# Kernel optimization log

Hardware: AMD Instinct MI355X
Metric: run time of the kernel (lower is better)

Reference implementation:

```python
import jax, jax.numpy as jnp
import numpy as np


def setup_inputs() -> dict:
    key = jax.random.key(0)
    k1, k2 = jax.random.split(key)
    x = jax.random.normal(k1, (32, 256, 56, 56), dtype=jnp.float32)
    conv_w = jax.random.normal(k2, (1, 2, 7, 7), dtype=jnp.float32) * 0.1
    return {"x": x, "conv_w": conv_w}


def reference(x, conv_w):
    # channel-wise mean and max, keepdim -> [B,1,H,W] each
    avg_out = jnp.mean(x, axis=1, keepdims=True)
    max_out = jnp.max(x, axis=1, keepdims=True)
    y = jnp.concatenate([avg_out, max_out], axis=1)  # [B,2,H,W]
    pad = (conv_w.shape[-1] - 1) // 2
    y = jax.lax.conv_general_dilated(
        y, conv_w,
        window_strides=(1, 1),
        padding=[(pad, pad), (pad, pad)],
        dimension_numbers=("NCHW", "OIHW", "NCHW"),
    )  # [B,1,H,W]
    y = jax.nn.sigmoid(y)
    return x * y
```

## Files before the change

### kernel.cpp

```cpp
#include <hip/hip_runtime.h>
#include <math.h>

#define BN   32
#define CN   256
#define HN   56
#define WN   56
#define HWN  (HN * WN)
#define HW4  (HWN / 4)
#define CHW4 (CN * HW4)
#define CHWN (CN * HWN)
#define NPOS (BN * HWN)
#define NQ   (NPOS / 4)

typedef float f32x4 __attribute__((ext_vector_type(4)));

__global__ __launch_bounds__(512) void sa_reduce_kernel(const f32x4* __restrict__ x4,
                                                        f32x4* __restrict__ avg4,
                                                        f32x4* __restrict__ mx4) {
    __shared__ f32x4 s_sum[16][32];
    __shared__ f32x4 s_max[16][32];

    int t    = threadIdx.x;
    int lane = t & 63;
    int w    = t >> 6;
    int j    = lane & 31;
    int sub  = lane >> 5;

    int q  = blockIdx.x * 32 + j;
    int b  = q / HW4;
    int s4 = q - b * HW4;
    const f32x4* xp = x4 + (size_t)b * CHW4 + (size_t)(w * 32 + sub) * HW4 + s4;

    f32x4 sum = {0.0f, 0.0f, 0.0f, 0.0f};
    f32x4 m   = {-INFINITY, -INFINITY, -INFINITY, -INFINITY};
#pragma unroll
    for (int k = 0; k < 16; ++k) {
        f32x4 v = xp[(size_t)(2 * k) * HW4];
        sum += v;
        m.x = fmaxf(m.x, v.x);
        m.y = fmaxf(m.y, v.y);
        m.z = fmaxf(m.z, v.z);
        m.w = fmaxf(m.w, v.w);
    }
    s_sum[w * 2 + sub][j] = sum;
    s_max[w * 2 + sub][j] = m;
    __syncthreads();

    if (t < 32) {
        f32x4 sa = s_sum[0][t];
        f32x4 ma = s_max[0][t];
#pragma unroll
        for (int p = 1; p < 16; ++p) {
            sa += s_sum[p][t];
            f32x4 mp = s_max[p][t];
            ma.x = fmaxf(ma.x, mp.x);
            ma.y = fmaxf(ma.y, mp.y);
            ma.z = fmaxf(ma.z, mp.z);
            ma.w = fmaxf(ma.w, mp.w);
        }
        int qq = blockIdx.x * 32 + t;
        avg4[qq] = sa * (1.0f / (float)CN);
        mx4[qq]  = ma;
    }
}

__global__ __launch_bounds__(256) void sa_conv_kernel(const float* __restrict__ avg,
                                                      const float* __restrict__ mx,
                                                      const float* __restrict__ cw,
                                                      float* __restrict__ att) {
    int p = blockIdx.x * blockDim.x + threadIdx.x;
    if (p >= NPOS) return;
    int b = p / HWN;
    int s = p - b * HWN;
    int h = s / WN;
    int w = s - h * WN;
    const float* a0 = avg + b * HWN;
    const float* m0 = mx + b * HWN;
    float acc = 0.0f;
#pragma unroll
    for (int kh = 0; kh < 7; ++kh) {
        int hh = h + kh - 3;
        if (hh < 0 || hh >= HN) continue;
#pragma unroll
        for (int kw = 0; kw < 7; ++kw) {
            int ww = w + kw - 3;
            if (ww < 0 || ww >= WN) continue;
            int idx = hh * WN + ww;
            acc = fmaf(cw[kh * 7 + kw],      a0[idx], acc);
            acc = fmaf(cw[49 + kh * 7 + kw], m0[idx], acc);
        }
    }
    att[p] = 1.0f / (1.0f + expf(-acc));
}

__global__ __launch_bounds__(256) void sa_mul_kernel(const f32x4* __restrict__ x4,
                                                     const f32x4* __restrict__ att4,
                                                     f32x4* __restrict__ out4) {
    int b = blockIdx.y;
    int i = blockIdx.x * 256 + threadIdx.x;
    int sq = i % HW4;
    f32x4 a = att4[(size_t)b * HW4 + sq];
    size_t gi = (size_t)b * CHW4 + i;
    f32x4 v = x4[gi];
    v *= a;
    __builtin_nontemporal_store(v, out4 + gi);
}

extern "C" void kernel_launch(void* const* d_in, const int* in_sizes, int n_in,
                              void* d_out, int out_size, void* d_ws, size_t ws_size,
                              hipStream_t stream) {
    const float* x  = (const float*)d_in[0];
    const float* cw = (const float*)d_in[1];
    float* out = (float*)d_out;

    float* avg = (float*)d_ws;
    float* mx  = avg + NPOS;
    float* att = mx + NPOS;

    {
        sa_reduce_kernel<<<NQ / 32, 512, 0, stream>>>(
            (const f32x4*)x, (f32x4*)avg, (f32x4*)mx);
    }
    {
        int blocks = (NPOS + 255) / 256;
        sa_conv_kernel<<<blocks, 256, 0, stream>>>(avg, mx, cw, att);
    }
    {
        dim3 grid(CHW4 / 256, BN);
        sa_mul_kernel<<<grid, 256, 0, stream>>>(
            (const f32x4*)x, (const f32x4*)att, (f32x4*)out);
    }
}
```

Measured before the change: 203.2 us.

## Fuse reduce, conv and multiply into one cooperative persistent kernel

Replaces three kernel launches with a single cooperative kernel of 784 blocks that performs the channel reduction, then a grid sync, the 7x7 conv plus sigmoid, then another grid sync, and finally the scaling multiply. Each block re-reads the same x positions it reduced, so the multiply pass may hit in L2 or the large last-level cache. This removes launch gaps between kernels. In exchange it adds two grid-wide barriers, and it needs all 784 blocks of 256 threads resident at once, which the 4-blocks-per-CU launch bound is meant to allow.

```diff
diff --git a/kernel.cpp b/kernel.cpp
--- a/kernel.cpp
+++ b/kernel.cpp
@@ -1,5 +1,8 @@
 #include <hip/hip_runtime.h>
+#include <hip/hip_cooperative_groups.h>
 #include <math.h>
+
+namespace cg = cooperative_groups;
 
 #define BN   32
 #define CN   256
@@ -11,14 +14,20 @@
 #define CHWN (CN * HWN)
 #define NPOS (BN * HWN)
 #define NQ   (NPOS / 4)
+#define GRID 784
 
 typedef float f32x4 __attribute__((ext_vector_type(4)));
 
-__global__ __launch_bounds__(512) void sa_reduce_kernel(const f32x4* __restrict__ x4,
-                                                        f32x4* __restrict__ avg4,
-                                                        f32x4* __restrict__ mx4) {
-    __shared__ f32x4 s_sum[16][32];
-    __shared__ f32x4 s_max[16][32];
+__global__ __launch_bounds__(256, 4) void sa_fused_kernel(
+    const f32x4* __restrict__ x4,
+    const float* __restrict__ cw,
+    f32x4*       __restrict__ out4,
+    float*       __restrict__ avg,
+    float*       __restrict__ mx,
+    float*       __restrict__ att)
+{
+    __shared__ f32x4 s_sum[8][32];
+    __shared__ f32x4 s_max[8][32];
 
     int t    = threadIdx.x;
     int lane = t & 63;
@@ -29,13 +38,13 @@
     int q  = blockIdx.x * 32 + j;
     int b  = q / HW4;
     int s4 = q - b * HW4;
-    const f32x4* xp = x4 + (size_t)b * CHW4 + (size_t)(w * 32 + sub) * HW4 + s4;
+    size_t xbase = (size_t)b * CHW4 + (size_t)(w * 64 + sub) * HW4 + s4;
 
     f32x4 sum = {0.0f, 0.0f, 0.0f, 0.0f};
     f32x4 m   = {-INFINITY, -INFINITY, -INFINITY, -INFINITY};
-#pragma unroll
-    for (int k = 0; k < 16; ++k) {
-        f32x4 v = xp[(size_t)(2 * k) * HW4];
+#pragma unroll 8
+    for (int k = 0; k < 32; ++k) {
+        f32x4 v = x4[xbase + (size_t)(2 * k) * HW4];
         sum += v;
         m.x = fmaxf(m.x, v.x);
         m.y = fmaxf(m.y, v.y);
@@ -50,7 +59,7 @@
         f32x4 sa = s_sum[0][t];
         f32x4 ma = s_max[0][t];
 #pragma unroll
-        for (int p = 1; p < 16; ++p) {
+        for (int p = 1; p < 8; ++p) {
             sa += s_sum[p][t];
             f32x4 mp = s_max[p][t];
             ma.x = fmaxf(ma.x, mp.x);
@@ -59,75 +68,65 @@
             ma.w = fmaxf(ma.w, mp.w);
         }
         int qq = blockIdx.x * 32 + t;
-        avg4[qq] = sa * (1.0f / (float)CN);
-        mx4[qq]  = ma;
+        ((f32x4*)avg)[qq] = sa * (1.0f / (float)CN);
+        ((f32x4*)mx)[qq]  = ma;
     }
-}
+    __threadfence();
+    cg::this_grid().sync();
 
-__global__ __launch_bounds__(256) void sa_conv_kernel(const float* __restrict__ avg,
-                                                      const float* __restrict__ mx,
-                                                      const float* __restrict__ cw,
-                                                      float* __restrict__ att) {
-    int p = blockIdx.x * blockDim.x + threadIdx.x;
-    if (p >= NPOS) return;
-    int b = p / HWN;
-    int s = p - b * HWN;
-    int h = s / WN;
-    int w = s - h * WN;
-    const float* a0 = avg + b * HWN;
-    const float* m0 = mx + b * HWN;
-    float acc = 0.0f;
+    if (t < 128) {
+        int p  = blockIdx.x * 128 + t;
+        int bb = p / HWN;
+        int s  = p - bb * HWN;
+        int h  = s / WN;
+        int w0 = s - h * WN;
+        const float* a0 = avg + bb * HWN;
+        const float* m0 = mx + bb * HWN;
+        float acc = 0.0f;
 #pragma unroll
-    for (int kh = 0; kh < 7; ++kh) {
-        int hh = h + kh - 3;
-        if (hh < 0 || hh >= HN) continue;
+        for (int kh = 0; kh < 7; ++kh) {
+            int hh = h + kh - 3;
+            if (hh < 0 || hh >= HN) continue;
 #pragma unroll
-        for (int kw = 0; kw < 7; ++kw) {
-            int ww = w + kw - 3;
-            if (ww < 0 || ww >= WN) continue;
-            int idx = hh * WN + ww;
-            acc = fmaf(cw[kh * 7 + kw],      a0[idx], acc);
-            acc = fmaf(cw[49 + kh * 7 + kw], m0[idx], acc);
+            for (int kw = 0; kw < 7; ++kw) {
+                int ww = w0 + kw - 3;
+                if (ww < 0 || ww >= WN) continue;
+                int idx = hh * WN + ww;
+                acc = fmaf(cw[kh * 7 + kw],      a0[idx], acc);
+                acc = fmaf(cw[49 + kh * 7 + kw], m0[idx], acc);
+            }
         }
+        att[p] = 1.0f / (1.0f + expf(-acc));
     }
-    att[p] = 1.0f / (1.0f + expf(-acc));
-}
+    __threadfence();
+    cg::this_grid().sync();
 
-__global__ __launch_bounds__(256) void sa_mul_kernel(const f32x4* __restrict__ x4,
-                                                     const f32x4* __restrict__ att4,
-                                                     f32x4* __restrict__ out4) {
-    int b = blockIdx.y;
-    int i = blockIdx.x * 256 + threadIdx.x;
-    int sq = i % HW4;
-    f32x4 a = att4[(size_t)b * HW4 + sq];
-    size_t gi = (size_t)b * CHW4 + i;
-    f32x4 v = x4[gi];
-    v *= a;
-    __builtin_nontemporal_store(v, out4 + gi);
+    f32x4 a = ((const f32x4*)att)[q];
+#pragma unroll 8
+    for (int k = 0; k < 32; ++k) {
+        size_t gi = xbase + (size_t)(2 * k) * HW4;
+        f32x4 v = x4[gi];
+        v.x *= a.x;
+        v.y *= a.y;
+        v.z *= a.z;
+        v.w *= a.w;
+        __builtin_nontemporal_store(v, out4 + gi);
+    }
 }
 
 extern "C" void kernel_launch(void* const* d_in, const int* in_sizes, int n_in,
                               void* d_out, int out_size, void* d_ws, size_t ws_size,
                               hipStream_t stream) {
-    const float* x  = (const float*)d_in[0];
-    const float* cw = (const float*)d_in[1];
-    float* out = (float*)d_out;
+    const f32x4* x4  = (const f32x4*)d_in[0];
+    const float* cw  = (const float*)d_in[1];
+    f32x4* out4      = (f32x4*)d_out;
 
     float* avg = (float*)d_ws;
     float* mx  = avg + NPOS;
     float* att = mx + NPOS;
 
-    {
-        sa_reduce_kernel<<<NQ / 32, 512, 0, stream>>>(
-            (const f32x4*)x, (f32x4*)avg, (f32x4*)mx);
-    }
-    {
-        int blocks = (NPOS + 255) / 256;
-        sa_conv_kernel<<<blocks, 256, 0, stream>>>(avg, mx, cw, att);
-    }
-    {
-        dim3 grid(CHW4 / 256, BN);
-        sa_mul_kernel<<<grid, 256, 0, stream>>>(
-            (const f32x4*)x, (const f32x4*)att, (f32x4*)out);
-    }
+    void* args[] = { (void*)&x4, (void*)&cw, (void*)&out4,
+                     (void*)&avg, (void*)&mx, (void*)&att };
+    hipLaunchCooperativeKernel((void*)sa_fused_kernel,
+                               dim3(GRID), dim3(256), args, 0, stream);
 }
```

Result: slower. 573.8 us (+182.4%).

## Widen reduce span to 64 positions and restructure multiply to loop over channels

Applied to the files above, without the earlier changes.

The reduce kernel now covers 64 float4 positions per block with 8 waves, and each wave reads 32 consecutive channels instead of interleaving two half-waves. The multiply kernel is rebuilt to match: each block loads its attention values once into shared memory, and each thread loops over 32 channels, replacing the previous one-element-per-thread grid. This is meant to make wave accesses fully contiguous, cut redundant attention loads and reduce block count. The trade-off is fewer blocks with more serial work per thread, which may lower memory-level parallelism.

```diff
diff --git a/kernel.cpp b/kernel.cpp
--- a/kernel.cpp
+++ b/kernel.cpp
@@ -8,49 +8,49 @@
 #define HWN  (HN * WN)
 #define HW4  (HWN / 4)
 #define CHW4 (CN * HW4)
-#define CHWN (CN * HWN)
 #define NPOS (BN * HWN)
 #define NQ   (NPOS / 4)
+#define SPAN 64
+#define NBLK (NQ / SPAN)
 
 typedef float f32x4 __attribute__((ext_vector_type(4)));
+
 
 __global__ __launch_bounds__(512) void sa_reduce_kernel(const f32x4* __restrict__ x4,
                                                         f32x4* __restrict__ avg4,
                                                         f32x4* __restrict__ mx4) {
-    __shared__ f32x4 s_sum[16][32];
-    __shared__ f32x4 s_max[16][32];
+    __shared__ f32x4 s_sum[8][SPAN];
+    __shared__ f32x4 s_max[8][SPAN];
 
-    int t    = threadIdx.x;
-    int lane = t & 63;
-    int w    = t >> 6;
-    int j    = lane & 31;
-    int sub  = lane >> 5;
+    int t = threadIdx.x;
+    int j = t & 63;
+    int w = t >> 6;
 
-    int q  = blockIdx.x * 32 + j;
+    int q  = blockIdx.x * SPAN + j;
     int b  = q / HW4;
     int s4 = q - b * HW4;
-    const f32x4* xp = x4 + (size_t)b * CHW4 + (size_t)(w * 32 + sub) * HW4 + s4;
+    const f32x4* xp = x4 + (size_t)b * CHW4 + (size_t)(w * 32) * HW4 + s4;
 
     f32x4 sum = {0.0f, 0.0f, 0.0f, 0.0f};
     f32x4 m   = {-INFINITY, -INFINITY, -INFINITY, -INFINITY};
-#pragma unroll
-    for (int k = 0; k < 16; ++k) {
-        f32x4 v = xp[(size_t)(2 * k) * HW4];
+#pragma unroll 8
+    for (int k = 0; k < 32; ++k) {
+        f32x4 v = xp[(size_t)k * HW4];
         sum += v;
         m.x = fmaxf(m.x, v.x);
         m.y = fmaxf(m.y, v.y);
         m.z = fmaxf(m.z, v.z);
         m.w = fmaxf(m.w, v.w);
     }
-    s_sum[w * 2 + sub][j] = sum;
-    s_max[w * 2 + sub][j] = m;
+    s_sum[w][j] = sum;
+    s_max[w][j] = m;
     __syncthreads();
 
-    if (t < 32) {
+    if (t < SPAN) {
         f32x4 sa = s_sum[0][t];
         f32x4 ma = s_max[0][t];
 #pragma unroll
-        for (int p = 1; p < 16; ++p) {
+        for (int p = 1; p < 8; ++p) {
             sa += s_sum[p][t];
             f32x4 mp = s_max[p][t];
             ma.x = fmaxf(ma.x, mp.x);
@@ -58,7 +58,7 @@
             ma.z = fmaxf(ma.z, mp.z);
             ma.w = fmaxf(ma.w, mp.w);
         }
-        int qq = blockIdx.x * 32 + t;
+        int qq = blockIdx.x * SPAN + t;
         avg4[qq] = sa * (1.0f / (float)CN);
         mx4[qq]  = ma;
     }
@@ -93,17 +93,33 @@
     att[p] = 1.0f / (1.0f + expf(-acc));
 }
 
-__global__ __launch_bounds__(256) void sa_mul_kernel(const f32x4* __restrict__ x4,
+__global__ __launch_bounds__(512) void sa_mul_kernel(const f32x4* __restrict__ x4,
                                                      const f32x4* __restrict__ att4,
                                                      f32x4* __restrict__ out4) {
-    int b = blockIdx.y;
-    int i = blockIdx.x * 256 + threadIdx.x;
-    int sq = i % HW4;
-    f32x4 a = att4[(size_t)b * HW4 + sq];
-    size_t gi = (size_t)b * CHW4 + i;
-    f32x4 v = x4[gi];
-    v *= a;
-    __builtin_nontemporal_store(v, out4 + gi);
+    __shared__ f32x4 s_att[SPAN];
+    int t = threadIdx.x;
+    int j = t & 63;
+    int w = t >> 6;
+
+    if (t < SPAN) s_att[t] = att4[blockIdx.x * SPAN + t];
+    __syncthreads();
+
+    int q  = blockIdx.x * SPAN + j;
+    int b  = q / HW4;
+    int s4 = q - b * HW4;
+    size_t base = (size_t)b * CHW4 + (size_t)(w * 32) * HW4 + s4;
+
+    f32x4 a = s_att[j];
+#pragma unroll 8
+    for (int k = 0; k < 32; ++k) {
+        size_t gi = base + (size_t)k * HW4;
+        f32x4 v = x4[gi];
+        v.x *= a.x;
+        v.y *= a.y;
+        v.z *= a.z;
+        v.w *= a.w;
+        __builtin_nontemporal_store(v, out4 + gi);
+    }
 }
 
 extern "C" void kernel_launch(void* const* d_in, const int* in_sizes, int n_in,
@@ -117,17 +133,11 @@
     float* mx  = avg + NPOS;
     float* att = mx + NPOS;
 
-    {
-        sa_reduce_kernel<<<NQ / 32, 512, 0, stream>>>(
-            (const f32x4*)x, (f32x4*)avg, (f32x4*)mx);
-    }
-    {
-        int blocks = (NPOS + 255) / 256;
-        sa_conv_kernel<<<blocks, 256, 0, stream>>>(avg, mx, cw, att);
-    }
-    {
-        dim3 grid(CHW4 / 256, BN);
-        sa_mul_kernel<<<grid, 256, 0, stream>>>(
-            (const f32x4*)x, (const f32x4*)att, (f32x4*)out);
-    }
+    sa_reduce_kernel<<<NBLK, 512, 0, stream>>>(
+        (const f32x4*)x, (f32x4*)avg, (f32x4*)mx);
+
+    sa_conv_kernel<<<(NPOS + 255) / 256, 256, 0, stream>>>(avg, mx, cw, att);
+
+    sa_mul_kernel<<<NBLK, 512, 0, stream>>>(
+        (const f32x4*)x, (const f32x4*)att, (f32x4*)out);
 }
```

New measurement: 204.8 us. No clear change (+0.8%).
